# Optimization experiments

Measured on AMD Instinct MI355X. Metric: run time of the kernel, lower is better.

The kernel has to match this reference:

```python
import jax, jax.numpy as jnp
import numpy as np

NUM_USERS = 50000
EMBED_DIM = 128
NUM_EDGES = 800000


def setup_inputs() -> dict:
    key = jax.random.key(0)
    k1, k2, k3, k4, k5 = jax.random.split(key, 5)
    user_emb = jax.random.normal(k1, (NUM_USERS, EMBED_DIM), dtype=jnp.float32)
    # xavier_uniform init for the square weight
    limit = float(np.sqrt(6.0 / (EMBED_DIM + EMBED_DIM)))
    social_weight = jax.random.uniform(k2, (EMBED_DIM, EMBED_DIM), dtype=jnp.float32,
                                       minval=-limit, maxval=limit)
    rows = jax.random.randint(k3, (NUM_EDGES,), 0, NUM_USERS)  # destination nodes
    cols = jax.random.randint(k4, (NUM_EDGES,), 0, NUM_USERS)  # source nodes
    vals = jax.random.uniform(k5, (NUM_EDGES,), dtype=jnp.float32)  # adjacency weights
    return {"user_emb": user_emb, "social_weight": social_weight,
            "rows": rows, "cols": cols, "vals": vals}


def reference(user_emb, social_weight, rows, cols, vals):
    # weighted_emb = user_emb @ W  (dense GEMM)
    weighted = jnp.matmul(user_emb, social_weight)  # [N, D]
    # neighbor_emb = sparse.mm(adj, weighted): out[i] = sum_{e: rows[e]==i} vals[e] * weighted[cols[e]]
    gathered = weighted[cols] * vals[:, None]  # [E, D]
    neighbor = jax.ops.segment_sum(gathered, rows, num_segments=user_emb.shape[0])  # [N, D]
    # dropout is identity in eval mode; residual add
    return user_emb + neighbor
```

## Files before the change

### kernel.cpp

```cpp
#include <hip/hip_runtime.h>

#define DD 128
#define CAP 32
#define OVF_MAX 4096
#define EPB 2048
#define BSHIFT 10
#define NBKT_MAX 64
#define BCAP 24576

typedef __attribute__((ext_vector_type(8))) short short8;
typedef __attribute__((ext_vector_type(8))) unsigned short u16x8;
typedef __attribute__((ext_vector_type(4))) float f32x4;

static __device__ __forceinline__ unsigned pack_bf16_2(float lo, float hi) {
  return __builtin_amdgcn_perm(__float_as_uint(hi) + 0x8000u,
                               __float_as_uint(lo) + 0x8000u, 0x07060302u);
}
static __device__ __forceinline__ unsigned short f2bf(float f) {
  return (unsigned short)((__float_as_uint(f) + 0x8000u) >> 16);
}
static __device__ __forceinline__ float bf2f(unsigned short h) {
  return __uint_as_float((unsigned)h << 16);
}

__global__ __launch_bounds__(256) void p1_bucket(
    const float* __restrict__ W, unsigned short* __restrict__ Wtg,
    const int* __restrict__ rows, const int* __restrict__ cols,
    const float* __restrict__ vals, int* __restrict__ binctr,
    int2* __restrict__ bucket, int* __restrict__ ovf_cnt,
    int4* __restrict__ ovf, int E, int nbkt) {
  const int t = threadIdx.x;
  if (blockIdx.x == 0) {
    const int k0 = (t >> 4) * 8;
    const int n0 = (t & 15) * 8;
    float v[8][8];
#pragma unroll
    for (int kk = 0; kk < 8; ++kk) {
      float4 a = *(const float4*)(W + (k0 + kk) * DD + n0);
      float4 b = *(const float4*)(W + (k0 + kk) * DD + n0 + 4);
      v[kk][0] = a.x; v[kk][1] = a.y; v[kk][2] = a.z; v[kk][3] = a.w;
      v[kk][4] = b.x; v[kk][5] = b.y; v[kk][6] = b.z; v[kk][7] = b.w;
    }
#pragma unroll
    for (int nn = 0; nn < 8; ++nn) {
      uint4 d;
      d.x = pack_bf16_2(v[0][nn], v[1][nn]);
      d.y = pack_bf16_2(v[2][nn], v[3][nn]);
      d.z = pack_bf16_2(v[4][nn], v[5][nn]);
      d.w = pack_bf16_2(v[6][nn], v[7][nn]);
      *(uint4*)(Wtg + (size_t)(n0 + nn) * DD + k0) = d;
    }
    return;
  }

  __shared__ int lrow[EPB];
  __shared__ int hist[NBKT_MAX];
  __shared__ int gbase[NBKT_MAX];
  __shared__ int lcur[NBKT_MAX];

  const int c0 = (blockIdx.x - 1) * EPB;
  const int n = min(EPB, E - c0);

  if (t < NBKT_MAX) { hist[t] = 0; lcur[t] = 0; }
  __syncthreads();

  for (int i = t; i < n; i += 256) {
    const int r = rows[c0 + i];
    lrow[i] = r;
    atomicAdd(&hist[r >> BSHIFT], 1);
  }
  __syncthreads();

  if (t < nbkt && hist[t] > 0) gbase[t] = atomicAdd(&binctr[t], hist[t]);
  __syncthreads();

  for (int i = t; i < n; i += 256) {
    const int r = lrow[i];
    const int b = r >> BSHIFT;
    const int lpos = atomicAdd(&lcur[b], 1);
    const int idx = gbase[b] + lpos;
    const int col = cols[c0 + i];
    const float v = vals[c0 + i];
    if (idx < BCAP) {
      bucket[(size_t)b * BCAP + idx] =
          make_int2(((r & 1023) << 22) | col, __float_as_int(v));
    } else {
      const int o = atomicAdd(ovf_cnt, 1);
      if (o < OVF_MAX) ovf[o] = make_int4(r, col, __float_as_int(v), 0);
    }
  }
}

#define WTS 136
__global__ __launch_bounds__(256) void p2k2_fused(
    const int* __restrict__ binctr, const int2* __restrict__ bucket,
    int* __restrict__ counts, int2* __restrict__ spair,
    int* __restrict__ ovf_cnt, int4* __restrict__ ovf,
    const float* __restrict__ U, const unsigned short* __restrict__ Wtg,
    unsigned short* __restrict__ wb, float* __restrict__ out, int N,
    int nbkt, int do_copy) {
  __shared__ union {
    unsigned short Wt[DD][WTS];
    int scnt[1 << BSHIFT];
  } sm;
  const int t = threadIdx.x;

  if ((int)blockIdx.x < nbkt) {
    const int b = blockIdx.x;
    const int base = b << BSHIFT;
    const int nrows = min(1 << BSHIFT, N - base);
    for (int i = t; i < (1 << BSHIFT); i += 256) sm.scnt[i] = 0;
    __syncthreads();

    const int nb = min(binctr[b], BCAP);
    const int2* __restrict__ bkt = bucket + (size_t)b * BCAP;
    for (int i = t; i < nb; i += 256) {
      const int2 p = bkt[i];
      const int lr = (unsigned)p.x >> 22;
      const int col = p.x & 0x3FFFFF;
      const int slot = atomicAdd(&sm.scnt[lr], 1);
      if (slot < CAP) {
        spair[(size_t)(base + lr) * CAP + slot] = make_int2(col, p.y);
      } else {
        const int o = atomicAdd(ovf_cnt, 1);
        if (o < OVF_MAX) ovf[o] = make_int4(base + lr, col, p.y, 0);
      }
    }
    __syncthreads();
    for (int i = t; i < nrows; i += 256) counts[base + i] = sm.scnt[i];
    return;
  }

  const int gb = blockIdx.x - nbkt;
#pragma unroll
  for (int i = 0; i < 8; ++i) {
    const int s = t + 256 * i;
    const int nn = s >> 4;
    const int k0 = (s & 15) * 8;
    uint4 d = *(const uint4*)(Wtg + (size_t)nn * DD + k0);
    *(uint4*)(&sm.Wt[nn][k0]) = d;
  }

  const int blk_row0 = gb * 128;
  if (do_copy) {
    const int nrow = min(128, N - blk_row0);
    const float4* U4 = (const float4*)(U + (size_t)blk_row0 * DD);
    float4* O4 = (float4*)(out + (size_t)blk_row0 * DD);
    for (int i = t; i < nrow * 32; i += 256) O4[i] = U4[i];
  }
  __syncthreads();

  const int w = t >> 6;
  const int lane = t & 63;
  const int m = lane & 15;
  const int quad = lane >> 4;
  const int row_base = blk_row0 + w * 32;

  short8 afrag[2][4];
#pragma unroll
  for (int s = 0; s < 2; ++s) {
    const int r = min(row_base + s * 16 + m, N - 1);
    const float* up = U + (size_t)r * DD + quad * 8;
#pragma unroll
    for (int c = 0; c < 4; ++c) {
      float4 x = *(const float4*)(up + c * 32);
      float4 y = *(const float4*)(up + c * 32 + 4);
      union { unsigned u[4]; short8 v; } fr;
      fr.u[0] = pack_bf16_2(x.x, x.y);
      fr.u[1] = pack_bf16_2(x.z, x.w);
      fr.u[2] = pack_bf16_2(y.x, y.y);
      fr.u[3] = pack_bf16_2(y.z, y.w);
      afrag[s][c] = fr.v;
    }
  }

  f32x4 acc[2][8];
#pragma unroll
  for (int s = 0; s < 2; ++s)
#pragma unroll
    for (int ct = 0; ct < 8; ++ct) acc[s][ct] = (f32x4){0.f, 0.f, 0.f, 0.f};

#pragma unroll
  for (int c = 0; c < 4; ++c) {
#pragma unroll
    for (int ct = 0; ct < 8; ++ct) {
      short8 bfrag = *(const short8*)&sm.Wt[ct * 16 + m][c * 32 + quad * 8];
      acc[0][ct] = __builtin_amdgcn_mfma_f32_16x16x32_bf16(
          afrag[0][c], bfrag, acc[0][ct], 0, 0, 0);
      acc[1][ct] = __builtin_amdgcn_mfma_f32_16x16x32_bf16(
          afrag[1][c], bfrag, acc[1][ct], 0, 0, 0);
    }
  }

#pragma unroll
  for (int s = 0; s < 2; ++s) {
    const int rb = row_base + s * 16 + quad * 4;
#pragma unroll
    for (int ct = 0; ct < 8; ++ct) {
#pragma unroll
      for (int reg = 0; reg < 4; ++reg) {
        const int r = rb + reg;
        if (r < N) wb[(size_t)r * DD + ct * 16 + m] = f2bf(acc[s][ct][reg]);
      }
    }
  }
}

__global__ __launch_bounds__(256) void k3_accumulate(
    const int* __restrict__ counts, const int2* __restrict__ spair,
    const unsigned short* __restrict__ wb, const float* __restrict__ U,
    const int* __restrict__ ovf_cnt, const int4* __restrict__ ovf,
    float* __restrict__ out, int N) {
  const int r = blockIdx.x * 4 + (threadIdx.x >> 6);
  if (r >= N) return;
  const int lane = threadIdx.x & 63;
  const int g = lane >> 4;
  const int sl = lane & 15;

  const u16x8* __restrict__ WB8 = (const u16x8*)wb;

  float acc[8];
#pragma unroll
  for (int d = 0; d < 8; ++d) acc[d] = 0.f;

  const int cnt = min(counts[r], CAP);
  const int2* __restrict__ lst = spair + (size_t)r * CAP;

  int i = 0;
  for (; i + 16 <= cnt; i += 16) {
    const int2 p0 = lst[i + g];
    const int2 p1 = lst[i + 4 + g];
    const int2 p2 = lst[i + 8 + g];
    const int2 p3 = lst[i + 12 + g];
    const u16x8 a0 = WB8[(size_t)p0.x * 16 + sl];
    const u16x8 a1 = WB8[(size_t)p1.x * 16 + sl];
    const u16x8 a2 = WB8[(size_t)p2.x * 16 + sl];
    const u16x8 a3 = WB8[(size_t)p3.x * 16 + sl];
    const float v0 = __int_as_float(p0.y);
    const float v1 = __int_as_float(p1.y);
    const float v2 = __int_as_float(p2.y);
    const float v3 = __int_as_float(p3.y);
#pragma unroll
    for (int d = 0; d < 8; ++d) {
      acc[d] = fmaf(v0, bf2f((unsigned short)a0[d]), acc[d]);
      acc[d] = fmaf(v1, bf2f((unsigned short)a1[d]), acc[d]);
      acc[d] = fmaf(v2, bf2f((unsigned short)a2[d]), acc[d]);
      acc[d] = fmaf(v3, bf2f((unsigned short)a3[d]), acc[d]);
    }
  }

  const int rem = cnt - i;
  if (rem > 8) {
    const int e0 = i + g, e1 = i + 4 + g, e2 = i + 8 + g, e3 = i + 12 + g;
    const int2 p0 = lst[min(e0, cnt - 1)];
    const int2 p1 = lst[min(e1, cnt - 1)];
    const int2 p2 = lst[min(e2, cnt - 1)];
    const int2 p3 = lst[min(e3, cnt - 1)];
    const u16x8 a0 = WB8[(size_t)p0.x * 16 + sl];
    const u16x8 a1 = WB8[(size_t)p1.x * 16 + sl];
    const u16x8 a2 = WB8[(size_t)p2.x * 16 + sl];
    const u16x8 a3 = WB8[(size_t)p3.x * 16 + sl];
    const float v0 = (e0 < cnt) ? __int_as_float(p0.y) : 0.f;
    const float v1 = (e1 < cnt) ? __int_as_float(p1.y) : 0.f;
    const float v2 = (e2 < cnt) ? __int_as_float(p2.y) : 0.f;
    const float v3 = (e3 < cnt) ? __int_as_float(p3.y) : 0.f;
#pragma unroll
    for (int d = 0; d < 8; ++d) {
      acc[d] = fmaf(v0, bf2f((unsigned short)a0[d]), acc[d]);
      acc[d] = fmaf(v1, bf2f((unsigned short)a1[d]), acc[d]);
      acc[d] = fmaf(v2, bf2f((unsigned short)a2[d]), acc[d]);
      acc[d] = fmaf(v3, bf2f((unsigned short)a3[d]), acc[d]);
    }
  } else if (rem > 0) {
    const int e0 = i + g, e1 = i + 4 + g;
    const int2 p0 = lst[min(e0, cnt - 1)];
    const int2 p1 = lst[min(e1, cnt - 1)];
    const u16x8 a0 = WB8[(size_t)p0.x * 16 + sl];
    const u16x8 a1 = WB8[(size_t)p1.x * 16 + sl];
    const float v0 = (e0 < cnt) ? __int_as_float(p0.y) : 0.f;
    const float v1 = (e1 < cnt) ? __int_as_float(p1.y) : 0.f;
#pragma unroll
    for (int d = 0; d < 8; ++d) {
      acc[d] = fmaf(v0, bf2f((unsigned short)a0[d]), acc[d]);
      acc[d] = fmaf(v1, bf2f((unsigned short)a1[d]), acc[d]);
    }
  }

#pragma unroll
  for (int d = 0; d < 8; ++d) {
    acc[d] += __shfl_xor(acc[d], 16, 64);
    acc[d] += __shfl_xor(acc[d], 32, 64);
  }

  const int nov = min(*ovf_cnt, OVF_MAX);
  if (nov > 0 && lane < 16) {
    for (int o = 0; o < nov; ++o) {
      const int4 e = ovf[o];
      if (e.x == r) {
        const float v = __int_as_float(e.z);
        const u16x8 a = WB8[(size_t)e.y * 16 + sl];
#pragma unroll
        for (int d = 0; d < 8; ++d)
          acc[d] = fmaf(v, bf2f((unsigned short)a[d]), acc[d]);
      }
    }
  }

  if (lane < 16) {
    const float* up = U + (size_t)r * DD + sl * 8;
    const float4 u0 = *(const float4*)up;
    const float4 u1 = *(const float4*)(up + 4);
    float4 o0, o1;
    o0.x = acc[0] + u0.x; o0.y = acc[1] + u0.y;
    o0.z = acc[2] + u0.z; o0.w = acc[3] + u0.w;
    o1.x = acc[4] + u1.x; o1.y = acc[5] + u1.y;
    o1.z = acc[6] + u1.z; o1.w = acc[7] + u1.w;
    float* op = out + (size_t)r * DD + sl * 8;
    *(float4*)op = o0;
    *(float4*)(op + 4) = o1;
  }
}

__global__ __launch_bounds__(256) void scatter_kernel(
    const int* __restrict__ rows, const int* __restrict__ cols,
    const float* __restrict__ vals, const unsigned short* __restrict__ wb,
    float* __restrict__ out, int E) {
  const int tid = blockIdx.x * 256 + threadIdx.x;
  const int e = tid >> 6;
  if (e >= E) return;
  const int lane = tid & 63;

  const int row = rows[e];
  const int col = cols[e];
  const float v = vals[e];

  const ushort2 w = ((const ushort2*)wb)[(size_t)col * 64 + lane];
  float* dst = out + (size_t)row * DD + lane * 2;
  unsafeAtomicAdd(dst, v * bf2f(w.x));
  unsafeAtomicAdd(dst + 1, v * bf2f(w.y));
}

static inline size_t align_up(size_t x, size_t a) { return (x + a - 1) & ~(a - 1); }

extern "C" void kernel_launch(void* const* d_in, const int* in_sizes, int n_in,
                              void* d_out, int out_size, void* d_ws, size_t ws_size,
                              hipStream_t stream) {
  const float* U = (const float*)d_in[0];
  const float* W = (const float*)d_in[1];
  const int* rows = (const int*)d_in[2];
  const int* cols = (const int*)d_in[3];
  const float* vals = (const float*)d_in[4];
  float* out = (float*)d_out;

  const int N = in_sizes[0] / DD;
  const int E = in_sizes[2];
  const int gemmBlocks = (N + 127) / 128;
  const int nchunks = (E + EPB - 1) / EPB;
  const int nbkt = (N + (1 << BSHIFT) - 1) >> BSHIFT;

  char* ws = (char*)d_ws;
  size_t off = 0;
  unsigned short* wb = (unsigned short*)(ws + off);
  off = align_up(off + (size_t)N * DD * sizeof(unsigned short), 16);
  unsigned short* Wtg = (unsigned short*)(ws + off);
  off = align_up(off + (size_t)DD * DD * sizeof(unsigned short), 16);
  int* counts = (int*)(ws + off);
  off = align_up(off + (size_t)N * sizeof(int), 16);
  int* binctr = (int*)(ws + off);
  int* ovf_cnt = binctr + NBKT_MAX;
  off = align_up(off + (NBKT_MAX + 4) * sizeof(int), 16);
  int4* ovf = (int4*)(ws + off);
  off = align_up(off + (size_t)OVF_MAX * sizeof(int4), 16);
  int2* bucket = (int2*)(ws + off);
  off = align_up(off + (size_t)nbkt * BCAP * sizeof(int2), 16);
  int2* spair = (int2*)(ws + off);
  off = align_up(off + (size_t)N * CAP * sizeof(int2), 16);
  const bool fast_ok = (off <= ws_size) && (nbkt <= NBKT_MAX);

  if (fast_ok) {
    hipMemsetAsync(binctr, 0, (NBKT_MAX + 1) * sizeof(int), stream);
    p1_bucket<<<1 + nchunks, 256, 0, stream>>>(
        W, Wtg, rows, cols, vals, binctr, bucket, ovf_cnt, ovf, E, nbkt);
    p2k2_fused<<<nbkt + gemmBlocks, 256, 0, stream>>>(
        binctr, bucket, counts, spair, ovf_cnt, ovf, U, Wtg, wb, out, N,
        nbkt, 0);
    k3_accumulate<<<(N + 3) / 4, 256, 0, stream>>>(
        counts, spair, wb, U, ovf_cnt, ovf, out, N);
  } else {
    p1_bucket<<<1, 256, 0, stream>>>(W, Wtg, rows, cols, vals, (int*)Wtg,
                                     (int2*)Wtg, (int*)Wtg, (int4*)Wtg, 0, 0);
    p2k2_fused<<<gemmBlocks, 256, 0, stream>>>(
        (const int*)Wtg, (const int2*)Wtg, (int*)Wtg, (int2*)Wtg, (int*)Wtg,
        (int4*)Wtg, U, Wtg, wb, out, N, 0, 1);
    const long long total = (long long)E * 64;
    scatter_kernel<<<(int)((total + 255) / 256), 256, 0, stream>>>(
        rows, cols, vals, wb, out, E);
  }
}
```

Measured before the change: 161.9 us.

## Use fine 64-row buckets with in-LDS sort and fuse bucketing into GEMM launch

Replaces the three-kernel pipeline (coarse 1024-row bucketing, per-row spair scatter plus GEMM, per-row accumulate) with two kernels. Edge bucketing into 64-row buckets now runs in the same launch as the GEMM, and each GEMM block transposes W itself instead of reading a pre-transposed copy. A second kernel sorts each bucket by row in LDS and accumulates directly, which drops the spair/counts global round-trip and one launch. In exchange, the GEMM blocks each redo the W conversion, the LDS union is larger, and the single-thread prefix scan and serialized row loop per block could limit parallelism.

```diff
diff --git a/kernel.cpp b/kernel.cpp
--- a/kernel.cpp
+++ b/kernel.cpp
@@ -4,9 +4,10 @@
 #define CAP 32
 #define OVF_MAX 4096
 #define EPB 2048
-#define BSHIFT 10
-#define NBKT_MAX 64
-#define BCAP 24576
+#define BSH 6
+#define NB2 800
+#define BC2 1408
+#define WTS 136
 
 typedef __attribute__((ext_vector_type(8))) short short8;
 typedef __attribute__((ext_vector_type(8))) unsigned short u16x8;
@@ -23,14 +24,63 @@
   return __uint_as_float((unsigned)h << 16);
 }
 
-__global__ __launch_bounds__(256) void p1_bucket(
-    const float* __restrict__ W, unsigned short* __restrict__ Wtg,
+__global__ __launch_bounds__(256) void kA_scatter_gemm(
+    const float* __restrict__ U, const float* __restrict__ W,
     const int* __restrict__ rows, const int* __restrict__ cols,
     const float* __restrict__ vals, int* __restrict__ binctr,
     int2* __restrict__ bucket, int* __restrict__ ovf_cnt,
-    int4* __restrict__ ovf, int E, int nbkt) {
+    int4* __restrict__ ovf, unsigned short* __restrict__ wb,
+    int N, int E, int nchunks, int nbkt) {
+  __shared__ union {
+    struct {
+      int lrow[EPB];
+      int hist[NB2];
+      int gbase[NB2];
+      int lcur[NB2];
+    } p1;
+    unsigned short Wt[DD][WTS];
+  } sm;
   const int t = threadIdx.x;
-  if (blockIdx.x == 0) {
+
+  if ((int)blockIdx.x < nchunks) {
+    const int c0 = blockIdx.x * EPB;
+    const int n = min(EPB, E - c0);
+
+    for (int j = t; j < nbkt; j += 256) { sm.p1.hist[j] = 0; sm.p1.lcur[j] = 0; }
+    __syncthreads();
+
+    for (int i = t; i < n; i += 256) {
+      const int r = rows[c0 + i];
+      sm.p1.lrow[i] = r;
+      atomicAdd(&sm.p1.hist[r >> BSH], 1);
+    }
+    __syncthreads();
+
+    for (int j = t; j < nbkt; j += 256)
+      if (sm.p1.hist[j] > 0)
+        sm.p1.gbase[j] = atomicAdd(&binctr[j], sm.p1.hist[j]);
+    __syncthreads();
+
+    for (int i = t; i < n; i += 256) {
+      const int r = sm.p1.lrow[i];
+      const int b = r >> BSH;
+      const int lpos = atomicAdd(&sm.p1.lcur[b], 1);
+      const int idx = sm.p1.gbase[b] + lpos;
+      const int col = cols[c0 + i];
+      const float v = vals[c0 + i];
+      if (idx < BC2) {
+        bucket[(size_t)b * BC2 + idx] =
+            make_int2(((r & 63) << 22) | col, __float_as_int(v));
+      } else {
+        const int o = atomicAdd(ovf_cnt, 1);
+        if (o < OVF_MAX) ovf[o] = make_int4(r, col, __float_as_int(v), 0);
+      }
+    }
+    return;
+  }
+
+  const int gb = blockIdx.x - nchunks;
+  {
     const int k0 = (t >> 4) * 8;
     const int n0 = (t & 15) * 8;
     float v[8][8];
@@ -48,108 +98,12 @@
       d.y = pack_bf16_2(v[2][nn], v[3][nn]);
       d.z = pack_bf16_2(v[4][nn], v[5][nn]);
       d.w = pack_bf16_2(v[6][nn], v[7][nn]);
-      *(uint4*)(Wtg + (size_t)(n0 + nn) * DD + k0) = d;
-    }
-    return;
-  }
-
-  __shared__ int lrow[EPB];
-  __shared__ int hist[NBKT_MAX];
-  __shared__ int gbase[NBKT_MAX];
-  __shared__ int lcur[NBKT_MAX];
-
-  const int c0 = (blockIdx.x - 1) * EPB;
-  const int n = min(EPB, E - c0);
-
-  if (t < NBKT_MAX) { hist[t] = 0; lcur[t] = 0; }
-  __syncthreads();
-
-  for (int i = t; i < n; i += 256) {
-    const int r = rows[c0 + i];
-    lrow[i] = r;
-    atomicAdd(&hist[r >> BSHIFT], 1);
-  }
-  __syncthreads();
-
-  if (t < nbkt && hist[t] > 0) gbase[t] = atomicAdd(&binctr[t], hist[t]);
-  __syncthreads();
-
-  for (int i = t; i < n; i += 256) {
-    const int r = lrow[i];
-    const int b = r >> BSHIFT;
-    const int lpos = atomicAdd(&lcur[b], 1);
-    const int idx = gbase[b] + lpos;
-    const int col = cols[c0 + i];
-    const float v = vals[c0 + i];
-    if (idx < BCAP) {
-      bucket[(size_t)b * BCAP + idx] =
-          make_int2(((r & 1023) << 22) | col, __float_as_int(v));
-    } else {
-      const int o = atomicAdd(ovf_cnt, 1);
-      if (o < OVF_MAX) ovf[o] = make_int4(r, col, __float_as_int(v), 0);
-    }
-  }
-}
-
-#define WTS 136
-__global__ __launch_bounds__(256) void p2k2_fused(
-    const int* __restrict__ binctr, const int2* __restrict__ bucket,
-    int* __restrict__ counts, int2* __restrict__ spair,
-    int* __restrict__ ovf_cnt, int4* __restrict__ ovf,
-    const float* __restrict__ U, const unsigned short* __restrict__ Wtg,
-    unsigned short* __restrict__ wb, float* __restrict__ out, int N,
-    int nbkt, int do_copy) {
-  __shared__ union {
-    unsigned short Wt[DD][WTS];
-    int scnt[1 << BSHIFT];
-  } sm;
-  const int t = threadIdx.x;
-
-  if ((int)blockIdx.x < nbkt) {
-    const int b = blockIdx.x;
-    const int base = b << BSHIFT;
-    const int nrows = min(1 << BSHIFT, N - base);
-    for (int i = t; i < (1 << BSHIFT); i += 256) sm.scnt[i] = 0;
-    __syncthreads();
-
-    const int nb = min(binctr[b], BCAP);
-    const int2* __restrict__ bkt = bucket + (size_t)b * BCAP;
-    for (int i = t; i < nb; i += 256) {
-      const int2 p = bkt[i];
-      const int lr = (unsigned)p.x >> 22;
-      const int col = p.x & 0x3FFFFF;
-      const int slot = atomicAdd(&sm.scnt[lr], 1);
-      if (slot < CAP) {
-        spair[(size_t)(base + lr) * CAP + slot] = make_int2(col, p.y);
-      } else {
-        const int o = atomicAdd(ovf_cnt, 1);
-        if (o < OVF_MAX) ovf[o] = make_int4(base + lr, col, p.y, 0);
-      }
-    }
-    __syncthreads();
-    for (int i = t; i < nrows; i += 256) counts[base + i] = sm.scnt[i];
-    return;
-  }
-
-  const int gb = blockIdx.x - nbkt;
-#pragma unroll
-  for (int i = 0; i < 8; ++i) {
-    const int s = t + 256 * i;
-    const int nn = s >> 4;
-    const int k0 = (s & 15) * 8;
-    uint4 d = *(const uint4*)(Wtg + (size_t)nn * DD + k0);
-    *(uint4*)(&sm.Wt[nn][k0]) = d;
-  }
+      *(uint4*)(&sm.Wt[n0 + nn][k0]) = d;
+    }
+  }
+  __syncthreads();
 
   const int blk_row0 = gb * 128;
-  if (do_copy) {
-    const int nrow = min(128, N - blk_row0);
-    const float4* U4 = (const float4*)(U + (size_t)blk_row0 * DD);
-    float4* O4 = (float4*)(out + (size_t)blk_row0 * DD);
-    for (int i = t; i < nrow * 32; i += 256) O4[i] = U4[i];
-  }
-  __syncthreads();
-
   const int w = t >> 6;
   const int lane = t & 63;
   const int m = lane & 15;
@@ -206,118 +160,263 @@
   }
 }
 
-__global__ __launch_bounds__(256) void k3_accumulate(
-    const int* __restrict__ counts, const int2* __restrict__ spair,
+__global__ __launch_bounds__(256) void kB_sort_accumulate(
+    const int* __restrict__ binctr, const int2* __restrict__ bucket,
     const unsigned short* __restrict__ wb, const float* __restrict__ U,
     const int* __restrict__ ovf_cnt, const int4* __restrict__ ovf,
     float* __restrict__ out, int N) {
-  const int r = blockIdx.x * 4 + (threadIdx.x >> 6);
-  if (r >= N) return;
-  const int lane = threadIdx.x & 63;
+  __shared__ int2 elist[BC2];
+  __shared__ int2 slist[BC2];
+  __shared__ int scnt[64];
+  __shared__ int sbase[64];
+  __shared__ int scur[64];
+
+  const int t = threadIdx.x;
+  const int b = blockIdx.x;
+  const int base = b << BSH;
+  const int n = min(binctr[b], BC2);
+
+  if (t < 64) scnt[t] = 0;
+  __syncthreads();
+
+  for (int i = t; i < n; i += 256) {
+    const int2 e = bucket[(size_t)b * BC2 + i];
+    elist[i] = e;
+    atomicAdd(&scnt[(unsigned)e.x >> 22], 1);
+  }
+  __syncthreads();
+
+  if (t == 0) {
+    int s = 0;
+#pragma unroll 1
+    for (int j = 0; j < 64; ++j) {
+      sbase[j] = s;
+      scur[j] = s;
+      s += scnt[j];
+    }
+  }
+  __syncthreads();
+
+  for (int i = t; i < n; i += 256) {
+    const int2 e = elist[i];
+    const int pos = atomicAdd(&scur[(unsigned)e.x >> 22], 1);
+    slist[pos] = make_int2(e.x & 0x3FFFFF, e.y);
+  }
+  __syncthreads();
+
+  const int lane = t & 63;
+  const int w = t >> 6;
   const int g = lane >> 4;
   const int sl = lane & 15;
-
   const u16x8* __restrict__ WB8 = (const u16x8*)wb;
-
-  float acc[8];
-#pragma unroll
-  for (int d = 0; d < 8; ++d) acc[d] = 0.f;
-
-  const int cnt = min(counts[r], CAP);
-  const int2* __restrict__ lst = spair + (size_t)r * CAP;
-
-  int i = 0;
-  for (; i + 16 <= cnt; i += 16) {
-    const int2 p0 = lst[i + g];
-    const int2 p1 = lst[i + 4 + g];
-    const int2 p2 = lst[i + 8 + g];
-    const int2 p3 = lst[i + 12 + g];
-    const u16x8 a0 = WB8[(size_t)p0.x * 16 + sl];
-    const u16x8 a1 = WB8[(size_t)p1.x * 16 + sl];
-    const u16x8 a2 = WB8[(size_t)p2.x * 16 + sl];
-    const u16x8 a3 = WB8[(size_t)p3.x * 16 + sl];
-    const float v0 = __int_as_float(p0.y);
-    const float v1 = __int_as_float(p1.y);
-    const float v2 = __int_as_float(p2.y);
-    const float v3 = __int_as_float(p3.y);
+  const int nov = min(*ovf_cnt, OVF_MAX);
+
+  for (int rl = w; rl < 64; rl += 4) {
+    const int r = base + rl;
+    if (r >= N) break;
+    const int cnt = scnt[rl];
+    const int st = sbase[rl];
+
+    float acc[8];
+#pragma unroll
+    for (int d = 0; d < 8; ++d) acc[d] = 0.f;
+
+    int i = 0;
+    for (; i + 16 <= cnt; i += 16) {
+      const int2 p0 = slist[st + i + g];
+      const int2 p1 = slist[st + i + 4 + g];
+      const int2 p2 = slist[st + i + 8 + g];
+      const int2 p3 = slist[st + i + 12 + g];
+      const u16x8 a0 = WB8[(size_t)p0.x * 16 + sl];
+      const u16x8 a1 = WB8[(size_t)p1.x * 16 + sl];
+      const u16x8 a2 = WB8[(size_t)p2.x * 16 + sl];
+      const u16x8 a3 = WB8[(size_t)p3.x * 16 + sl];
+      const float v0 = __int_as_float(p0.y);
+      const float v1 = __int_as_float(p1.y);
+      const float v2 = __int_as_float(p2.y);
+      const float v3 = __int_as_float(p3.y);
+#pragma unroll
+      for (int d = 0; d < 8; ++d) {
+        acc[d] = fmaf(v0, bf2f((unsigned short)a0[d]), acc[d]);
+        acc[d] = fmaf(v1, bf2f((unsigned short)a1[d]), acc[d]);
+        acc[d] = fmaf(v2, bf2f((unsigned short)a2[d]), acc[d]);
+        acc[d] = fmaf(v3, bf2f((unsigned short)a3[d]), acc[d]);
+      }
+    }
+
+    const int rem = cnt - i;
+    if (rem > 8) {
+      const int e0 = i + g, e1 = i + 4 + g, e2 = i + 8 + g, e3 = i + 12 + g;
+      const int2 p0 = slist[st + min(e0, cnt - 1)];
+      const int2 p1 = slist[st + min(e1, cnt - 1)];
+      const int2 p2 = slist[st + min(e2, cnt - 1)];
+      const int2 p3 = slist[st + min(e3, cnt - 1)];
+      const u16x8 a0 = WB8[(size_t)p0.x * 16 + sl];
+      const u16x8 a1 = WB8[(size_t)p1.x * 16 + sl];
+      const u16x8 a2 = WB8[(size_t)p2.x * 16 + sl];
+      const u16x8 a3 = WB8[(size_t)p3.x * 16 + sl];
+      const float v0 = (e0 < cnt) ? __int_as_float(p0.y) : 0.f;
+      const float v1 = (e1 < cnt) ? __int_as_float(p1.y) : 0.f;
+      const float v2 = (e2 < cnt) ? __int_as_float(p2.y) : 0.f;
+      const float v3 = (e3 < cnt) ? __int_as_float(p3.y) : 0.f;
+#pragma unroll
+      for (int d = 0; d < 8; ++d) {
+        acc[d] = fmaf(v0, bf2f((unsigned short)a0[d]), acc[d]);
+        acc[d] = fmaf(v1, bf2f((unsigned short)a1[d]), acc[d]);
+        acc[d] = fmaf(v2, bf2f((unsigned short)a2[d]), acc[d]);
+        acc[d] = fmaf(v3, bf2f((unsigned short)a3[d]), acc[d]);
+      }
+    } else if (rem > 0) {
+      const int e0 = i + g, e1 = i + 4 + g;
+      const int2 p0 = slist[st + min(e0, cnt - 1)];
+      const int2 p1 = slist[st + min(e1, cnt - 1)];
+      const u16x8 a0 = WB8[(size_t)p0.x * 16 + sl];
+      const u16x8 a1 = WB8[(size_t)p1.x * 16 + sl];
+      const float v0 = (e0 < cnt) ? __int_as_float(p0.y) : 0.f;
+      const float v1 = (e1 < cnt) ? __int_as_float(p1.y) : 0.f;
+#pragma unroll
+      for (int d = 0; d < 8; ++d) {
+        acc[d] = fmaf(v0, bf2f((unsigned short)a0[d]), acc[d]);
+        acc[d] = fmaf(v1, bf2f((unsigned short)a1[d]), acc[d]);
+      }
+    }
+
 #pragma unroll
     for (int d = 0; d < 8; ++d) {
-      acc[d] = fmaf(v0, bf2f((unsigned short)a0[d]), acc[d]);
-      acc[d] = fmaf(v1, bf2f((unsigned short)a1[d]), acc[d]);
-      acc[d] = fmaf(v2, bf2f((unsigned short)a2[d]), acc[d]);
-      acc[d] = fmaf(v3, bf2f((unsigned short)a3[d]), acc[d]);
-    }
-  }
-
-  const int rem = cnt - i;
-  if (rem > 8) {
-    const int e0 = i + g, e1 = i + 4 + g, e2 = i + 8 + g, e3 = i + 12 + g;
-    const int2 p0 = lst[min(e0, cnt - 1)];
-    const int2 p1 = lst[min(e1, cnt - 1)];
-    const int2 p2 = lst[min(e2, cnt - 1)];
-    const int2 p3 = lst[min(e3, cnt - 1)];
-    const u16x8 a0 = WB8[(size_t)p0.x * 16 + sl];
-    const u16x8 a1 = WB8[(size_t)p1.x * 16 + sl];
-    const u16x8 a2 = WB8[(size_t)p2.x * 16 + sl];
-    const u16x8 a3 = WB8[(size_t)p3.x * 16 + sl];
-    const float v0 = (e0 < cnt) ? __int_as_float(p0.y) : 0.f;
-    const float v1 = (e1 < cnt) ? __int_as_float(p1.y) : 0.f;
-    const float v2 = (e2 < cnt) ? __int_as_float(p2.y) : 0.f;
-    const float v3 = (e3 < cnt) ? __int_as_float(p3.y) : 0.f;
-#pragma unroll
-    for (int d = 0; d < 8; ++d) {
-      acc[d] = fmaf(v0, bf2f((unsigned short)a0[d]), acc[d]);
-      acc[d] = fmaf(v1, bf2f((unsigned short)a1[d]), acc[d]);
-      acc[d] = fmaf(v2, bf2f((unsigned short)a2[d]), acc[d]);
-      acc[d] = fmaf(v3, bf2f((unsigned short)a3[d]), acc[d]);
-    }
-  } else if (rem > 0) {
-    const int e0 = i + g, e1 = i + 4 + g;
-    const int2 p0 = lst[min(e0, cnt - 1)];
-    const int2 p1 = lst[min(e1, cnt - 1)];
-    const u16x8 a0 = WB8[(size_t)p0.x * 16 + sl];
-    const u16x8 a1 = WB8[(size_t)p1.x * 16 + sl];
-    const float v0 = (e0 < cnt) ? __int_as_float(p0.y) : 0.f;
-    const float v1 = (e1 < cnt) ? __int_as_float(p1.y) : 0.f;
-#pragma unroll
-    for (int d = 0; d < 8; ++d) {
-      acc[d] = fmaf(v0, bf2f((unsigned short)a0[d]), acc[d]);
-      acc[d] = fmaf(v1, bf2f((unsigned short)a1[d]), acc[d]);
-    }
-  }
-
-#pragma unroll
-  for (int d = 0; d < 8; ++d) {
-    acc[d] += __shfl_xor(acc[d], 16, 64);
-    acc[d] += __shfl_xor(acc[d], 32, 64);
-  }
-
-  const int nov = min(*ovf_cnt, OVF_MAX);
-  if (nov > 0 && lane < 16) {
-    for (int o = 0; o < nov; ++o) {
-      const int4 e = ovf[o];
-      if (e.x == r) {
-        const float v = __int_as_float(e.z);
-        const u16x8 a = WB8[(size_t)e.y * 16 + sl];
-#pragma unroll
-        for (int d = 0; d < 8; ++d)
-          acc[d] = fmaf(v, bf2f((unsigned short)a[d]), acc[d]);
-      }
-    }
-  }
-
-  if (lane < 16) {
-    const float* up = U + (size_t)r * DD + sl * 8;
-    const float4 u0 = *(const float4*)up;
-    const float4 u1 = *(const float4*)(up + 4);
-    float4 o0, o1;
-    o0.x = acc[0] + u0.x; o0.y = acc[1] + u0.y;
-    o0.z = acc[2] + u0.z; o0.w = acc[3] + u0.w;
-    o1.x = acc[4] + u1.x; o1.y = acc[5] + u1.y;
-    o1.z = acc[6] + u1.z; o1.w = acc[7] + u1.w;
-    float* op = out + (size_t)r * DD + sl * 8;
-    *(float4*)op = o0;
-    *(float4*)(op + 4) = o1;
+      acc[d] += __shfl_xor(acc[d], 16, 64);
+      acc[d] += __shfl_xor(acc[d], 32, 64);
+    }
+
+    if (nov > 0 && lane < 16) {
+      for (int o = 0; o < nov; ++o) {
+        const int4 e = ovf[o];
+        if (e.x == r) {
+          const float v = __int_as_float(e.z);
+          const u16x8 a = WB8[(size_t)e.y * 16 + sl];
+#pragma unroll
+          for (int d = 0; d < 8; ++d)
+            acc[d] = fmaf(v, bf2f((unsigned short)a[d]), acc[d]);
+        }
+      }
+    }
+
+    if (lane < 16) {
+      const float* up = U + (size_t)r * DD + sl * 8;
+      const float4 u0 = *(const float4*)up;
+      const float4 u1 = *(const float4*)(up + 4);
+      float4 o0, o1;
+      o0.x = acc[0] + u0.x; o0.y = acc[1] + u0.y;
+      o0.z = acc[2] + u0.z; o0.w = acc[3] + u0.w;
+      o1.x = acc[4] + u1.x; o1.y = acc[5] + u1.y;
+      o1.z = acc[6] + u1.z; o1.w = acc[7] + u1.w;
+      float* op = out + (size_t)r * DD + sl * 8;
+      *(float4*)op = o0;
+      *(float4*)(op + 4) = o1;
+    }
+  }
+}
+
+__global__ __launch_bounds__(256) void p1_bucket(
+    const float* __restrict__ W, unsigned short* __restrict__ Wtg,
+    int E) {
+  const int t = threadIdx.x;
+  const int k0 = (t >> 4) * 8;
+  const int n0 = (t & 15) * 8;
+  float v[8][8];
+#pragma unroll
+  for (int kk = 0; kk < 8; ++kk) {
+    float4 a = *(const float4*)(W + (k0 + kk) * DD + n0);
+    float4 b = *(const float4*)(W + (k0 + kk) * DD + n0 + 4);
+    v[kk][0] = a.x; v[kk][1] = a.y; v[kk][2] = a.z; v[kk][3] = a.w;
+    v[kk][4] = b.x; v[kk][5] = b.y; v[kk][6] = b.z; v[kk][7] = b.w;
+  }
+#pragma unroll
+  for (int nn = 0; nn < 8; ++nn) {
+    uint4 d;
+    d.x = pack_bf16_2(v[0][nn], v[1][nn]);
+    d.y = pack_bf16_2(v[2][nn], v[3][nn]);
+    d.z = pack_bf16_2(v[4][nn], v[5][nn]);
+    d.w = pack_bf16_2(v[6][nn], v[7][nn]);
+    *(uint4*)(Wtg + (size_t)(n0 + nn) * DD + k0) = d;
+  }
+}
+
+__global__ __launch_bounds__(256) void k2_gemm_copy(
+    const float* __restrict__ U, const unsigned short* __restrict__ Wtg,
+    unsigned short* __restrict__ wb, float* __restrict__ out, int N) {
+  __shared__ unsigned short Wt[DD][WTS];
+  const int t = threadIdx.x;
+  const int gb = blockIdx.x;
+#pragma unroll
+  for (int i = 0; i < 8; ++i) {
+    const int s = t + 256 * i;
+    const int nn = s >> 4;
+    const int k0 = (s & 15) * 8;
+    uint4 d = *(const uint4*)(Wtg + (size_t)nn * DD + k0);
+    *(uint4*)(&Wt[nn][k0]) = d;
+  }
+  const int blk_row0 = gb * 128;
+  {
+    const int nrow = min(128, N - blk_row0);
+    const float4* U4 = (const float4*)(U + (size_t)blk_row0 * DD);
+    float4* O4 = (float4*)(out + (size_t)blk_row0 * DD);
+    for (int i = t; i < nrow * 32; i += 256) O4[i] = U4[i];
+  }
+  __syncthreads();
+
+  const int w = t >> 6;
+  const int lane = t & 63;
+  const int m = lane & 15;
+  const int quad = lane >> 4;
+  const int row_base = blk_row0 + w * 32;
+
+  short8 afrag[2][4];
+#pragma unroll
+  for (int s = 0; s < 2; ++s) {
+    const int r = min(row_base + s * 16 + m, N - 1);
+    const float* up = U + (size_t)r * DD + quad * 8;
+#pragma unroll
+    for (int c = 0; c < 4; ++c) {
+      float4 x = *(const float4*)(up + c * 32);
+      float4 y = *(const float4*)(up + c * 32 + 4);
+      union { unsigned u[4]; short8 v; } fr;
+      fr.u[0] = pack_bf16_2(x.x, x.y);
+      fr.u[1] = pack_bf16_2(x.z, x.w);
+      fr.u[2] = pack_bf16_2(y.x, y.y);
+      fr.u[3] = pack_bf16_2(y.z, y.w);
+      afrag[s][c] = fr.v;
+    }
+  }
+
+  f32x4 acc[2][8];
+#pragma unroll
+  for (int s = 0; s < 2; ++s)
+#pragma unroll
+    for (int ct = 0; ct < 8; ++ct) acc[s][ct] = (f32x4){0.f, 0.f, 0.f, 0.f};
+
+#pragma unroll
+  for (int c = 0; c < 4; ++c) {
+#pragma unroll
+    for (int ct = 0; ct < 8; ++ct) {
+      short8 bfrag = *(const short8*)&Wt[ct * 16 + m][c * 32 + quad * 8];
+      acc[0][ct] = __builtin_amdgcn_mfma_f32_16x16x32_bf16(
+          afrag[0][c], bfrag, acc[0][ct], 0, 0, 0);
+      acc[1][ct] = __builtin_amdgcn_mfma_f32_16x16x32_bf16(
+          afrag[1][c], bfrag, acc[1][ct], 0, 0, 0);
+    }
+  }
+
+#pragma unroll
+  for (int s = 0; s < 2; ++s) {
+    const int rb = row_base + s * 16 + quad * 4;
+#pragma unroll
+    for (int ct = 0; ct < 8; ++ct) {
+#pragma unroll
+      for (int reg = 0; reg < 4; ++reg) {
+        const int r = rb + reg;
+        if (r < N) wb[(size_t)r * DD + ct * 16 + m] = f2bf(acc[s][ct][reg]);
+      }
+    }
   }
 }
 
@@ -356,7 +455,7 @@
   const int E = in_sizes[2];
   const int gemmBlocks = (N + 127) / 128;
   const int nchunks = (E + EPB - 1) / EPB;
-  const int nbkt = (N + (1 << BSHIFT) - 1) >> BSHIFT;
+  const int nbkt = (N + (1 << BSH) - 1) >> BSH;
 
   char* ws = (char*)d_ws;
   size_t off = 0;
@@ -364,34 +463,25 @@
   off = align_up(off + (size_t)N * DD * sizeof(unsigned short), 16);
   unsigned short* Wtg = (unsigned short*)(ws + off);
   off = align_up(off + (size_t)DD * DD * sizeof(unsigned short), 16);
-  int* counts = (int*)(ws + off);
-  off = align_up(off + (size_t)N * sizeof(int), 16);
   int* binctr = (int*)(ws + off);
-  int* ovf_cnt = binctr + NBKT_MAX;
-  off = align_up(off + (NBKT_MAX + 4) * sizeof(int), 16);
+  int* ovf_cnt = binctr + NB2;
+  off = align_up(off + (NB2 + 4) * sizeof(int), 16);
   int4* ovf = (int4*)(ws + off);
   off = align_up(off + (size_t)OVF_MAX * sizeof(int4), 16);
   int2* bucket = (int2*)(ws + off);
-  off = align_up(off + (size_t)nbkt * BCAP * sizeof(int2), 16);
-  int2* spair = (int2*)(ws + off);
-  off = align_up(off + (size_t)N * CAP * sizeof(int2), 16);
-  const bool fast_ok = (off <= ws_size) && (nbkt <= NBKT_MAX);
+  off = align_up(off + (size_t)nbkt * BC2 * sizeof(int2), 16);
+  const bool fast_ok = (off <= ws_size) && (nbkt <= NB2);
 
   if (fast_ok) {
-    hipMemsetAsync(binctr, 0, (NBKT_MAX + 1) * sizeof(int), stream);
-    p1_bucket<<<1 + nchunks, 256, 0, stream>>>(
-        W, Wtg, rows, cols, vals, binctr, bucket, ovf_cnt, ovf, E, nbkt);
-    p2k2_fused<<<nbkt + gemmBlocks, 256, 0, stream>>>(
-        binctr, bucket, counts, spair, ovf_cnt, ovf, U, Wtg, wb, out, N,
-        nbkt, 0);
-    k3_accumulate<<<(N + 3) / 4, 256, 0, stream>>>(
-        counts, spair, wb, U, ovf_cnt, ovf, out, N);
+    hipMemsetAsync(binctr, 0, (NB2 + 1) * sizeof(int), stream);
+    kA_scatter_gemm<<<nchunks + gemmBlocks, 256, 0, stream>>>(
+        U, W, rows, cols, vals, binctr, bucket, ovf_cnt, ovf, wb, N, E,
+        nchunks, nbkt);
+    kB_sort_accumulate<<<nbkt, 256, 0, stream>>>(
+        binctr, bucket, wb, U, ovf_cnt, ovf, out, N);
   } else {
-    p1_bucket<<<1, 256, 0, stream>>>(W, Wtg, rows, cols, vals, (int*)Wtg,
-                                     (int2*)Wtg, (int*)Wtg, (int4*)Wtg, 0, 0);
-    p2k2_fused<<<gemmBlocks, 256, 0, stream>>>(
-        (const int*)Wtg, (const int2*)Wtg, (int*)Wtg, (int2*)Wtg, (int*)Wtg,
-        (int4*)Wtg, U, Wtg, wb, out, N, 0, 1);
+    p1_bucket<<<1, 256, 0, stream>>>(W, Wtg, E);
+    k2_gemm_copy<<<gemmBlocks, 256, 0, stream>>>(U, Wtg, wb, out, N);
     const long long total = (long long)E * 64;
     scatter_kernel<<<(int)((total + 255) / 256), 256, 0, stream>>>(
         rows, cols, vals, wb, out, E);
```

After: 149.7 us. -7.5%, faster.
